# Optimization experiments

Measured on AMD Instinct MI355X. Metric: run time of the kernel, lower is better.

## Reference

```python
import jax, jax.numpy as jnp
import numpy as np
from jax.ops import segment_sum, segment_max

N = 400000          # points
V = 100000          # occupied voxels
EPS = 1e-3          # BN eps from norm_cfg
VX, VY, VZ = 0.2, 0.2, 4.0          # voxel_size
X0, Y0, Z0 = 0.0, -40.0, -3.0       # point_cloud_range mins
GX, GY, GZ = 352, 400, 1            # grid dims


def setup_inputs() -> dict:
    key = jax.random.key(0)
    ks = jax.random.split(key, 12)
    # points: xyz uniform inside the point cloud range, 4th channel = intensity
    xyz = jax.random.uniform(ks[0], (N, 3), jnp.float32) \
        * jnp.array([70.4, 80.0, 4.0], jnp.float32) \
        + jnp.array([X0, Y0, Z0], jnp.float32)
    inten = jax.random.uniform(ks[1], (N, 1), jnp.float32)
    features = jnp.concatenate([xyz, inten], axis=1)
    # point -> voxel mapping; guarantee every voxel id occupied so
    # segment_max semantics match torch's unique-voxel reduce exactly
    inv = jnp.concatenate([jnp.arange(V, dtype=jnp.int32),
                           jax.random.randint(ks[2], (N - V,), 0, V, jnp.int32)])
    inv = jax.random.permutation(ks[3], inv)
    # voxel coordinates (batch, z, y, x)
    b = jax.random.randint(ks[4], (V,), 0, 2, jnp.int32)
    z = jnp.zeros((V,), jnp.int32)
    y = jax.random.randint(ks[5], (V,), 0, GY, jnp.int32)
    x = jax.random.randint(ks[6], (V,), 0, GX, jnp.int32)
    coors = jnp.stack([b, z, y, x], axis=1)
    # VFE params: Linear(bias=False) + BN1d(gamma, beta)
    W0 = jax.random.normal(ks[7], (64, 10), jnp.float32) * (1.0 / np.sqrt(10))
    W1 = jax.random.normal(ks[8], (64, 128), jnp.float32) * (1.0 / np.sqrt(128))
    return dict(features=features, W0=W0,
                gamma0=jnp.ones((64,), jnp.float32), beta0=jnp.zeros((64,), jnp.float32),
                W1=W1,
                gamma1=jnp.ones((64,), jnp.float32), beta1=jnp.zeros((64,), jnp.float32),
                inv=inv, coors=coors)


def _bn_relu(x, gamma, beta):
    # BN1d in training mode: biased batch stats over the point dim
    mu = jnp.mean(x, axis=0)
    var = jnp.var(x, axis=0)
    return jax.nn.relu(gamma * (x - mu) * jax.lax.rsqrt(var + EPS) + beta)


def _stats(xyz, inv, coors):
    # cluster-center offset: per-voxel mean of xyz, gathered back
    cnt = segment_sum(jnp.ones((xyz.shape[0],), xyz.dtype), inv, num_segments=V)
    mean = segment_sum(xyz, inv, num_segments=V) / cnt[:, None]
    f_cluster = xyz - mean[inv]
    # voxel-center offset: coors order is (batch, z, y, x)
    cf = coors.astype(xyz.dtype)
    center = jnp.stack([cf[:, 3] * VX + VX / 2 + X0,
                        cf[:, 2] * VY + VY / 2 + Y0,
                        cf[:, 1] * VZ + VZ / 2 + Z0], axis=1)
    f_center = xyz - center[inv]
    return jnp.concatenate([xyz, f_cluster, f_center], axis=1)  # [N, 9]


def reference(features, W0, gamma0, beta0, W1, gamma1, beta1, inv, coors):
    x = jnp.concatenate([_stats(features[:, :3], inv, coors), features[:, 3:]], axis=1)  # [N,10]
    # VFE layer 0
    h0 = _bn_relu(x @ W0.T, gamma0, beta0)                     # [N,64]
    v0 = segment_max(h0, inv, num_segments=V)                  # [V,64]
    x1 = jnp.concatenate([h0, v0[inv]], axis=1)                # [N,128]
    # VFE layer 1
    h1 = _bn_relu(x1 @ W1.T, gamma1, beta1)                    # [N,64]
    voxel_feats = segment_max(h1, inv, num_segments=V)         # [V,64]
    return voxel_feats, coors
```

## Files before the change

### kernel.cpp

```cpp
#include <hip/hip_runtime.h>
#include <hip/hip_bf16.h>

#define NPTS 400000
#define NVOX 100000
#define EPSB 1e-3f
#define NTILE 6250
#define NBLK_SCAN 391
#define GBLK 782

#define OFF_ACC4   0
#define OFF_GRAM   (4*NVOX)
#define OFF_P1     (OFF_GRAM + 128)
#define ZERO_FLOATS (OFF_P1 + 4096)
#define OFF_V0     ZERO_FLOATS
#define OFF_Y1M    (OFF_V0 + NVOX*64)
#define OFF_VTMP   (OFF_Y1M + NVOX*64)
#define OFF_BSUM   (OFF_VTMP + NVOX)
#define OFF_VOFF   (OFF_BSUM + 512)
#define OFF_VSTART (OFF_VOFF + NVOX)
#define OFF_ORD    (OFF_VSTART + NVOX + 8)
#define OFF_VS     (OFF_ORD + NPTS)
#define OFF_W0F    (OFF_VS + NPTS)
#define OFF_W1B    (OFF_W0F + 640)
#define OFF_H0T    (OFF_W1B + 4096)

#define XTB_LD 136
#define HT_LD  65

typedef __bf16 bf16x8 __attribute__((ext_vector_type(8)));
typedef float  f32x4  __attribute__((ext_vector_type(4)));

__device__ __forceinline__ float b2f(__hip_bfloat16 h) { return __bfloat162float(h); }
__device__ __forceinline__ float bfbits2f(unsigned short u) {
    return __uint_as_float((unsigned int)u << 16);
}
__device__ __forceinline__ unsigned short bf16u(float f) {
    __hip_bfloat16 h = __float2bfloat16(f);
    return __builtin_bit_cast(unsigned short, h);
}
__device__ __forceinline__ unsigned int fkey(float f) {
    unsigned int u = __float_as_uint(f);
    return (u & 0x80000000u) ? ~u : (u | 0x80000000u);
}
__device__ __forceinline__ float funkey(unsigned int k) {
    unsigned int u = (k & 0x80000000u) ? (k & 0x7FFFFFFFu) : ~k;
    return __uint_as_float(u);
}

__device__ __forceinline__ void compute_x(const __hip_bfloat16* __restrict__ feat,
                                          const float* __restrict__ acc4,
                                          const int* __restrict__ coors,
                                          long i, int v, float* xv) {
    ushort4 f4 = *(const ushort4*)(feat + 4 * i);
    float px = bfbits2f(f4.x), py = bfbits2f(f4.y), pz = bfbits2f(f4.z), it = bfbits2f(f4.w);
    float4 a4 = *(const float4*)&acc4[4 * (long)v];
    float ic = 1.0f / a4.x;
    int4 c4 = *(const int4*)&coors[4 * (long)v];
    xv[0] = px; xv[1] = py; xv[2] = pz;
    xv[3] = px - a4.y * ic; xv[4] = py - a4.z * ic; xv[5] = pz - a4.w * ic;
    xv[6] = px - ((float)c4.w * 0.2f + 0.1f);
    xv[7] = py - ((float)c4.z * 0.2f + 0.1f - 40.0f);
    xv[8] = pz - ((float)c4.y * 4.0f + 2.0f - 3.0f);
    xv[9] = it;
}

__global__ void k_vsum(const __hip_bfloat16* __restrict__ feat,
                       const int* __restrict__ inv,
                       float* __restrict__ acc4,
                       const __hip_bfloat16* __restrict__ W0,
                       const __hip_bfloat16* __restrict__ W1,
                       float* __restrict__ W0f, unsigned short* __restrict__ w1b) {
    if (blockIdx.x == 6250) {
        int t = threadIdx.x;
        for (int j = t; j < 640; j += 256) W0f[j] = b2f(W0[j]);
        for (int f = t; f < 8192; f += 256) {
            int j  = f & 7;
            int l  = (f >> 3) & 63;
            int ks = (f >> 9) & 3;
            int ct = f >> 11;
            int ch = ct * 16 + (l & 15);
            int k  = ks * 32 + ((l >> 4) & 3) * 8 + j;
            w1b[f] = __builtin_bit_cast(unsigned short, W1[ch * 128 + k]);
        }
        return;
    }
    long t = (long)blockIdx.x * 256 + threadIdx.x;
    int pt = (int)(t >> 2);
    int comp = (int)(t & 3);
    float val = (comp == 0) ? 1.0f : b2f(feat[4 * pt + comp - 1]);
    int v = inv[pt];
    atomicAdd(&acc4[(long)v * 4 + comp], val);
}

__global__ void k_scan1(const float* __restrict__ acc4,
                        int* __restrict__ vtmp, int* __restrict__ bsum) {
    __shared__ int sc[256];
    int b = blockIdx.x, t = threadIdx.x;
    int v = b * 256 + t;
    int c = (v < NVOX) ? (int)acc4[4 * (long)v] : 0;
    sc[t] = c;
    __syncthreads();
    int val = c;
    for (int off = 1; off < 256; off <<= 1) {
        int x = (t >= off) ? sc[t - off] : 0;
        __syncthreads();
        val += x; sc[t] = val;
        __syncthreads();
    }
    if (v < NVOX) vtmp[v] = val - c;
    if (t == 255) bsum[b] = val;
}

__global__ void k_scan2(int* __restrict__ bsum) {
    __shared__ int sc[512];
    int t = threadIdx.x;
    int c = (t < NBLK_SCAN) ? bsum[t] : 0;
    sc[t] = c;
    __syncthreads();
    int val = c;
    for (int off = 1; off < 512; off <<= 1) {
        int x = (t >= off) ? sc[t - off] : 0;
        __syncthreads();
        val += x; sc[t] = val;
        __syncthreads();
    }
    if (t < NBLK_SCAN) bsum[t] = val - c;
}

__global__ void k_scan3(const int* __restrict__ vtmp, const int* __restrict__ bsum,
                        int* __restrict__ voff, int* __restrict__ vstart,
                        int* __restrict__ vsorted,
                        float* __restrict__ v0, unsigned int* __restrict__ y1m) {
    int v = blockIdx.x * 256 + threadIdx.x;
    if (v < NVOX) {
        int s0 = vtmp[v] + bsum[v >> 8];
        voff[v] = s0;
        vstart[v] = s0;
        int s1;
        if (v + 1 < NVOX) s1 = vtmp[v + 1] + bsum[(v + 1) >> 8];
        else              s1 = NPTS;
        for (int j = s0; j < s1; j++) vsorted[j] = v;
        if ((s0 >> 4) != ((s1 - 1) >> 4)) {
            float4 z4 = {0.f, 0.f, 0.f, 0.f};
            float4* pv = (float4*)&v0[(long)v * 64];
            float4* py = (float4*)&y1m[(long)v * 64];
#pragma unroll
            for (int u = 0; u < 16; u++) { pv[u] = z4; py[u] = z4; }
        }
    }
    if (v == 0) vstart[NVOX] = NPTS;
}

__global__ __launch_bounds__(256, 4)
void k_prep(const __hip_bfloat16* __restrict__ feat,
            const int* __restrict__ inv,
            const int* __restrict__ coors,
            const float* __restrict__ acc4,
            int* __restrict__ voff,
            int* __restrict__ ord,
            float* __restrict__ gram) {
    __shared__ float gs[72];
    int t = threadIdx.x;
    if (t < 72) gs[t] = 0.0f;
    __syncthreads();

    float sx[10], sxx[55];
#pragma unroll
    for (int a = 0; a < 10; a++) sx[a] = 0.0f;
#pragma unroll
    for (int a = 0; a < 55; a++) sxx[a] = 0.0f;

    for (long i = (long)blockIdx.x * 256 + t; i < NPTS; i += (long)GBLK * 256) {
        int v = inv[i];
        float xv[10];
        compute_x(feat, acc4, coors, i, v, xv);
        int idx = 0;
#pragma unroll
        for (int a = 0; a < 10; a++) {
            sx[a] += xv[a];
#pragma unroll
            for (int b = 0; b <= a; b++) sxx[idx++] += xv[a] * xv[b];
        }
        int pos = atomicAdd(&voff[v], 1);
        ord[pos] = (int)i;
    }

#pragma unroll
    for (int v = 0; v < 65; v++) {
        float s = (v < 10) ? sx[v] : sxx[v - 10];
        for (int m = 32; m >= 1; m >>= 1) s += __shfl_xor(s, m);
        if ((t & 63) == 0) atomicAdd(&gs[v], s);
    }
    __syncthreads();
    if (t < 65) atomicAdd(&gram[t], gs[t]);
}

__global__ __launch_bounds__(256, 6)
void k_h0max(const int* __restrict__ ord, const int* __restrict__ vsorted,
             const int* __restrict__ vstart,
             const __hip_bfloat16* __restrict__ feat,
             const float* __restrict__ acc4, const int* __restrict__ coors,
             const float* __restrict__ W0f, const float* __restrict__ gram,
             const __hip_bfloat16* __restrict__ g0,
             const __hip_bfloat16* __restrict__ be0,
             float* __restrict__ v0, unsigned short* __restrict__ h0t) {
    __shared__ float ht[64 * HT_LD];
    __shared__ int invs[64];
    __shared__ float sc0s[64], bi0s[64];
    int t = threadIdx.x, w = t >> 6, l = t & 63;
    int base = blockIdx.x * 64;
    int i = ord[base + l];
    int v = vsorted[base + l];
    if (w == 0) invs[l] = v;

    float xv[10];
    compute_x(feat, acc4, coors, (long)i, v, xv);

    if (w == 1) {
        int c = l;
        float wr[10];
#pragma unroll
        for (int k = 0; k < 10; k++) wr[k] = W0f[c * 10 + k];
        float sum = 0.0f, sq = 0.0f;
#pragma unroll
        for (int a = 0; a < 10; a++) {
            sum += wr[a] * gram[a];
            float ta = 0.0f;
#pragma unroll
            for (int b = 0; b < 10; b++) {
                int hi = (a >= b) ? a : b, lo = (a >= b) ? b : a;
                ta += wr[b] * gram[10 + hi * (hi + 1) / 2 + lo];
            }
            sq += wr[a] * ta;
        }
        float mu  = sum * (1.0f / NPTS);
        float var = sq * (1.0f / NPTS) - mu * mu;
        float g   = b2f(g0[c]) * rsqrtf(var + EPSB);
        sc0s[c] = g;
        bi0s[c] = b2f(be0[c]) - mu * g;
    }
    __syncthreads();

    int cw = w * 16;
#pragma unroll
    for (int j = 0; j < 16; j++) {
        int c = cw + j;
        float y = 0.0f;
#pragma unroll
        for (int k = 0; k < 10; k++) y += xv[k] * W0f[c*10 + k];
        ht[l * HT_LD + c] = fmaxf(sc0s[c] * y + bi0s[c], 0.0f);
    }
    __syncthreads();

#pragma unroll
    for (int u = 0; u < 2; u++) {
        int idx = t + u * 256;
        int pt2 = idx >> 3;
        int c0 = (idx & 7) * 8;
        const float* src = &ht[pt2 * HT_LD + c0];
        float4 a  = *(const float4*)src;
        float4 b4 = *(const float4*)(src + 4);
        uint4 o;
        o.x = (unsigned int)bf16u(a.x)  | ((unsigned int)bf16u(a.y)  << 16);
        o.y = (unsigned int)bf16u(a.z)  | ((unsigned int)bf16u(a.w)  << 16);
        o.z = (unsigned int)bf16u(b4.x) | ((unsigned int)bf16u(b4.y) << 16);
        o.w = (unsigned int)bf16u(b4.z) | ((unsigned int)bf16u(b4.w) << 16);
        *(uint4*)&h0t[(long)(base + pt2) * 64 + c0] = o;
    }

    unsigned int mk = 0u;
#pragma unroll
    for (int j = 0; j < 16; j++) {
        int p = cw + j;
        unsigned int hb = __float_as_uint(ht[p * HT_LD + l]);
        mk = (hb > mk) ? hb : mk;
        if (j == 15 || invs[p + 1] != invs[p]) {
            int vv = invs[p];
            int s0 = vstart[vv], s1 = vstart[vv + 1];
            unsigned int* dst = (unsigned int*)&v0[(long)vv * 64 + l];
            if (s0 >= base + cw && s1 <= base + cw + 16)
                *dst = mk;
            else
                atomicMax(dst, mk);
            mk = 0u;
        }
    }
}

__global__ __launch_bounds__(256, 6)
void k_mfma_stats(const int* __restrict__ vsorted,
                  const int* __restrict__ vstart,
                  const unsigned short* __restrict__ h0t,
                  const unsigned short* __restrict__ w1b,
                  const float* __restrict__ v0,
                  float* __restrict__ P1,
                  unsigned int* __restrict__ y1m) {
    __shared__ union {
        unsigned short xtb[64 * XTB_LD];
        float ht[64 * HT_LD];
    } sm;
    __shared__ int invs[64];
    int t = threadIdx.x, w = t >> 6, l = t & 63;
    int quad = l >> 4, lm = l & 15;
    int base = blockIdx.x * 64;
    if (w == 0) invs[l] = vsorted[base + l];

    bf16x8 bfrag[4];
    const uint4* wf = (const uint4*)w1b;
#pragma unroll
    for (int ks = 0; ks < 4; ks++)
        bfrag[ks] = __builtin_bit_cast(bf16x8, wf[(w * 4 + ks) * 64 + l]);

#pragma unroll
    for (int u = 0; u < 2; u++) {
        int idx = t + u * 256;
        int pt = idx >> 3, c0 = (idx & 7) * 8;
        uint4 d = *(const uint4*)&h0t[(long)(base + pt) * 64 + c0];
        *(uint4*)&sm.xtb[pt * XTB_LD + c0] = d;
    }
    {
        int p = t >> 2, q = t & 3;
        int vv = vsorted[base + p];
        const float4* src = (const float4*)&v0[(long)vv * 64 + q * 16];
#pragma unroll
        for (int u = 0; u < 4; u++) {
            float4 f4 = src[u];
            ushort4 s4 = { bf16u(f4.x), bf16u(f4.y), bf16u(f4.z), bf16u(f4.w) };
            *(ushort4*)&sm.xtb[p * XTB_LD + 64 + q * 16 + 4 * u] = s4;
        }
    }
    __syncthreads();

    f32x4 acc[4];
#pragma unroll
    for (int pg = 0; pg < 4; pg++) acc[pg] = (f32x4){0.f, 0.f, 0.f, 0.f};
#pragma unroll
    for (int ks = 0; ks < 4; ks++) {
#pragma unroll
        for (int pg = 0; pg < 4; pg++) {
            const uint4* ap = (const uint4*)&sm.xtb[(pg * 16 + lm) * XTB_LD + ks * 32 + quad * 8];
            bf16x8 a = __builtin_bit_cast(bf16x8, *ap);
            acc[pg] = __builtin_amdgcn_mfma_f32_16x16x32_bf16(a, bfrag[ks], acc[pg], 0, 0, 0);
        }
    }

    float ssum = 0.0f, ssq = 0.0f;
#pragma unroll
    for (int pg = 0; pg < 4; pg++) {
#pragma unroll
        for (int r = 0; r < 4; r++) {
            float y = acc[pg][r];
            ssum += y; ssq += y * y;
        }
    }
    __syncthreads();

#pragma unroll
    for (int pg = 0; pg < 4; pg++) {
#pragma unroll
        for (int r = 0; r < 4; r++)
            sm.ht[(pg * 16 + quad * 4 + r) * HT_LD + w * 16 + lm] = acc[pg][r];
    }
    __syncthreads();

    unsigned int mk = 0u;
    int cw = w * 16;
#pragma unroll
    for (int j = 0; j < 16; j++) {
        int p = cw + j;
        unsigned int k2 = fkey(sm.ht[p * HT_LD + l]);
        mk = (k2 > mk) ? k2 : mk;
        if (j == 15 || invs[p + 1] != invs[p]) {
            int vv = invs[p];
            int s0 = vstart[vv], s1 = vstart[vv + 1];
            unsigned int* dst = &y1m[(long)vv * 64 + l];
            if (s0 >= base + cw && s1 <= base + cw + 16)
                *dst = mk;
            else
                atomicMax(dst, mk);
            mk = 0u;
        }
    }

    ssum += __shfl_xor(ssum, 16); ssq += __shfl_xor(ssq, 16);
    ssum += __shfl_xor(ssum, 32); ssq += __shfl_xor(ssq, 32);
    if (l < 16) {
        int slot = blockIdx.x & 31;
        atomicAdd(&P1[slot * 128 + w * 16 + lm], ssum);
        atomicAdd(&P1[slot * 128 + 64 + w * 16 + lm], ssq);
    }
}

#define OUTBLK 512
__global__ __launch_bounds__(256)
void k_out(const unsigned int* __restrict__ y1m,
           const float* __restrict__ P1,
           const __hip_bfloat16* __restrict__ gamma,
           const __hip_bfloat16* __restrict__ beta,
           const int* __restrict__ coors,
           float* __restrict__ out) {
    __shared__ float sc1s[64], bi1s[64];
    int t = threadIdx.x;
    if (t < 64) {
        float sum = 0.0f, sq = 0.0f;
        for (int s = 0; s < 32; s++) {
            sum += P1[s*128 + t];
            sq  += P1[s*128 + 64 + t];
        }
        float mu  = sum * (1.0f / NPTS);
        float var = sq * (1.0f / NPTS) - mu * mu;
        float g   = b2f(gamma[t]) * rsqrtf(var + EPSB);
        sc1s[t] = g;
        bi1s[t] = b2f(beta[t]) - mu * g;
    }
    __syncthreads();

    const long n4feat = (long)NVOX * 16;
    const long n4all  = n4feat + NVOX;
    const long nfeat  = (long)NVOX * 64;
    for (long idx = (long)blockIdx.x * 256 + t; idx < n4all; idx += (long)OUTBLK * 256) {
        if (idx < n4feat) {
            uint4 kk = ((const uint4*)y1m)[idx];
            int c0 = (int)((idx * 4) & 63);
            float4 o;
            o.x = fmaxf(sc1s[c0+0] * funkey(kk.x) + bi1s[c0+0], 0.0f);
            o.y = fmaxf(sc1s[c0+1] * funkey(kk.y) + bi1s[c0+1], 0.0f);
            o.z = fmaxf(sc1s[c0+2] * funkey(kk.z) + bi1s[c0+2], 0.0f);
            o.w = fmaxf(sc1s[c0+3] * funkey(kk.w) + bi1s[c0+3], 0.0f);
            ((float4*)out)[idx] = o;
        } else {
            long vi = idx - n4feat;
            int4 c4 = ((const int4*)coors)[vi];
            float4 o;
            o.x = b2f(__float2bfloat16((float)c4.x));
            o.y = b2f(__float2bfloat16((float)c4.y));
            o.z = b2f(__float2bfloat16((float)c4.z));
            o.w = b2f(__float2bfloat16((float)c4.w));
            ((float4*)(out + nfeat))[vi] = o;
        }
    }
}

extern "C" void kernel_launch(void* const* d_in, const int* in_sizes, int n_in,
                              void* d_out, int out_size, void* d_ws, size_t ws_size,
                              hipStream_t stream) {
    const __hip_bfloat16* feat = (const __hip_bfloat16*)d_in[0];
    const __hip_bfloat16* W0   = (const __hip_bfloat16*)d_in[1];
    const __hip_bfloat16* g0   = (const __hip_bfloat16*)d_in[2];
    const __hip_bfloat16* be0  = (const __hip_bfloat16*)d_in[3];
    const __hip_bfloat16* W1   = (const __hip_bfloat16*)d_in[4];
    const __hip_bfloat16* g1   = (const __hip_bfloat16*)d_in[5];
    const __hip_bfloat16* be1  = (const __hip_bfloat16*)d_in[6];
    const int* inv   = (const int*)d_in[7];
    const int* coors = (const int*)d_in[8];
    float* out = (float*)d_out;

    float* ws    = (float*)d_ws;
    float* acc4  = ws + OFF_ACC4;
    float* gram  = ws + OFF_GRAM;
    float* P1    = ws + OFF_P1;
    float* v0    = ws + OFF_V0;
    unsigned int* y1m = (unsigned int*)(ws + OFF_Y1M);
    int* vtmp    = (int*)(ws + OFF_VTMP);
    int* bsum    = (int*)(ws + OFF_BSUM);
    int* voff    = (int*)(ws + OFF_VOFF);
    int* vstart  = (int*)(ws + OFF_VSTART);
    int* ord     = (int*)(ws + OFF_ORD);
    int* vsorted = (int*)(ws + OFF_VS);
    float* W0f   = ws + OFF_W0F;
    unsigned short* w1b = (unsigned short*)(ws + OFF_W1B);
    unsigned short* h0t = (unsigned short*)(ws + OFF_H0T);

    hipMemsetAsync(ws, 0, (size_t)ZERO_FLOATS * sizeof(float), stream);

    k_vsum<<<6251, 256, 0, stream>>>(feat, inv, acc4, W0, W1, W0f, w1b);
    k_scan1<<<NBLK_SCAN, 256, 0, stream>>>(acc4, vtmp, bsum);
    k_scan2<<<1, 512, 0, stream>>>(bsum);
    k_scan3<<<NBLK_SCAN, 256, 0, stream>>>(vtmp, bsum, voff, vstart, vsorted, v0, y1m);
    k_prep<<<GBLK, 256, 0, stream>>>(feat, inv, coors, acc4, voff, ord, gram);
    k_h0max<<<NTILE, 256, 0, stream>>>(ord, vsorted, vstart, feat, acc4, coors,
                                       W0f, gram, g0, be0, v0, h0t);
    k_mfma_stats<<<NTILE, 256, 0, stream>>>(vsorted, vstart, h0t, w1b, v0, P1, y1m);
    k_out<<<OUTBLK, 256, 0, stream>>>(y1m, P1, g1, be1, coors, out);
}
```

Measured before the change: 256.9 us.

## Decompose layer-0 Gram moments into per-point and per-voxel terms

After: 285.9 us. +11.3%, slower.

```diff
diff --git a/kernel.cpp b/kernel.cpp
--- a/kernel.cpp
+++ b/kernel.cpp
@@ -9,10 +9,13 @@
 #define GBLK 782
 
 #define OFF_ACC4   0
-#define OFF_GRAM   (4*NVOX)
-#define OFF_P1     (OFF_GRAM + 128)
+#define OFF_ACCI   (4*NVOX)
+#define OFF_AMOM   (5*NVOX)
+#define OFF_BMOM   (OFF_AMOM + 512)
+#define OFF_P1     (OFF_BMOM + 1024)
 #define ZERO_FLOATS (OFF_P1 + 4096)
-#define OFF_V0     ZERO_FLOATS
+#define OFF_STATS  ZERO_FLOATS
+#define OFF_V0     (OFF_STATS + 128)
 #define OFF_Y1M    (OFF_V0 + NVOX*64)
 #define OFF_VTMP   (OFF_Y1M + NVOX*64)
 #define OFF_BSUM   (OFF_VTMP + NVOX)
@@ -66,7 +69,7 @@
 
 __global__ void k_vsum(const __hip_bfloat16* __restrict__ feat,
                        const int* __restrict__ inv,
-                       float* __restrict__ acc4,
+                       float* __restrict__ acc4, float* __restrict__ accI,
                        const __hip_bfloat16* __restrict__ W0,
                        const __hip_bfloat16* __restrict__ W1,
                        float* __restrict__ W0f, unsigned short* __restrict__ w1b) {
@@ -87,9 +90,13 @@
     long t = (long)blockIdx.x * 256 + threadIdx.x;
     int pt = (int)(t >> 2);
     int comp = (int)(t & 3);
-    float val = (comp == 0) ? 1.0f : b2f(feat[4 * pt + comp - 1]);
     int v = inv[pt];
-    atomicAdd(&acc4[(long)v * 4 + comp], val);
+    if (comp == 0) {
+        atomicAdd(&acc4[(long)v * 4], 1.0f);
+        atomicAdd(&accI[v], b2f(feat[4 * pt + 3]));
+    } else {
+        atomicAdd(&acc4[(long)v * 4 + comp], b2f(feat[4 * pt + comp - 1]));
+    }
 }
 
 __global__ void k_scan1(const float* __restrict__ acc4,
@@ -154,45 +161,162 @@
 __global__ __launch_bounds__(256, 4)
 void k_prep(const __hip_bfloat16* __restrict__ feat,
             const int* __restrict__ inv,
-            const int* __restrict__ coors,
-            const float* __restrict__ acc4,
             int* __restrict__ voff,
             int* __restrict__ ord,
-            float* __restrict__ gram) {
-    __shared__ float gs[72];
+            float* __restrict__ amom) {
+    __shared__ float gs[16];
     int t = threadIdx.x;
-    if (t < 72) gs[t] = 0.0f;
-    __syncthreads();
-
-    float sx[10], sxx[55];
-#pragma unroll
-    for (int a = 0; a < 10; a++) sx[a] = 0.0f;
-#pragma unroll
-    for (int a = 0; a < 55; a++) sxx[a] = 0.0f;
+    if (t < 16) gs[t] = 0.0f;
+    __syncthreads();
+
+    float a[14];
+#pragma unroll
+    for (int k = 0; k < 14; k++) a[k] = 0.0f;
 
     for (long i = (long)blockIdx.x * 256 + t; i < NPTS; i += (long)GBLK * 256) {
+        ushort4 f4 = *(const ushort4*)(feat + 4 * i);
+        float px = bfbits2f(f4.x), py = bfbits2f(f4.y);
+        float pz = bfbits2f(f4.z), it = bfbits2f(f4.w);
+        a[0] += px;      a[1] += py;      a[2] += pz;
+        a[3] += px * px; a[4] += py * px; a[5] += py * py;
+        a[6] += pz * px; a[7] += pz * py; a[8] += pz * pz;
+        a[9] += it;      a[10] += it * px; a[11] += it * py; a[12] += it * pz;
+        a[13] += it * it;
         int v = inv[i];
-        float xv[10];
-        compute_x(feat, acc4, coors, i, v, xv);
-        int idx = 0;
-#pragma unroll
-        for (int a = 0; a < 10; a++) {
-            sx[a] += xv[a];
-#pragma unroll
-            for (int b = 0; b <= a; b++) sxx[idx++] += xv[a] * xv[b];
-        }
         int pos = atomicAdd(&voff[v], 1);
         ord[pos] = (int)i;
     }
 
 #pragma unroll
-    for (int v = 0; v < 65; v++) {
-        float s = (v < 10) ? sx[v] : sxx[v - 10];
+    for (int k = 0; k < 14; k++) {
+        float s = a[k];
         for (int m = 32; m >= 1; m >>= 1) s += __shfl_xor(s, m);
-        if ((t & 63) == 0) atomicAdd(&gs[v], s);
-    }
-    __syncthreads();
-    if (t < 65) atomicAdd(&gram[t], gs[t]);
+        if ((t & 63) == 0) atomicAdd(&gs[k], s);
+    }
+    __syncthreads();
+    if (t < 14) atomicAdd(&amom[(blockIdx.x & 31) * 16 + t], gs[t]);
+}
+
+__global__ void k_bmom(const float* __restrict__ acc4,
+                       const float* __restrict__ accI,
+                       const int* __restrict__ coors,
+                       float* __restrict__ bmom) {
+    __shared__ float gs[32];
+    int t = threadIdx.x;
+    if (t < 32) gs[t] = 0.0f;
+    __syncthreads();
+
+    int v = blockIdx.x * 256 + t;
+    float n = 0, sx = 0, sy = 0, sz = 0, I = 0, cx = 0, cy = 0, cz = 0, in = 0;
+    if (v < NVOX) {
+        float4 a4 = *(const float4*)&acc4[4 * (long)v];
+        n = a4.x; sx = a4.y; sy = a4.z; sz = a4.w;
+        I = accI[v];
+        int4 c4 = *(const int4*)&coors[4 * (long)v];
+        cx = (float)c4.w * 0.2f + 0.1f;
+        cy = (float)c4.z * 0.2f + 0.1f - 40.0f;
+        cz = (float)c4.y * 4.0f + 2.0f - 3.0f;
+        in = 1.0f / n;
+    }
+    float vals[30];
+    vals[0] = sx * sx * in; vals[1] = sy * sx * in; vals[2] = sy * sy * in;
+    vals[3] = sz * sx * in; vals[4] = sz * sy * in; vals[5] = sz * sz * in;
+    vals[6]  = sx * cx; vals[7]  = sx * cy; vals[8]  = sx * cz;
+    vals[9]  = sy * cx; vals[10] = sy * cy; vals[11] = sy * cz;
+    vals[12] = sz * cx; vals[13] = sz * cy; vals[14] = sz * cz;
+    vals[15] = n * cx * cx; vals[16] = n * cy * cx; vals[17] = n * cy * cy;
+    vals[18] = n * cz * cx; vals[19] = n * cz * cy; vals[20] = n * cz * cz;
+    vals[21] = n * cx; vals[22] = n * cy; vals[23] = n * cz;
+    vals[24] = I * sx * in; vals[25] = I * sy * in; vals[26] = I * sz * in;
+    vals[27] = I * cx; vals[28] = I * cy; vals[29] = I * cz;
+
+#pragma unroll
+    for (int k = 0; k < 30; k++) {
+        float s = vals[k];
+        for (int m = 32; m >= 1; m >>= 1) s += __shfl_xor(s, m);
+        if ((t & 63) == 0) atomicAdd(&gs[k], s);
+    }
+    __syncthreads();
+    if (t < 30) atomicAdd(&bmom[(blockIdx.x & 31) * 32 + t], gs[t]);
+}
+
+__global__ void k_gasm(const float* __restrict__ amom, const float* __restrict__ bmom,
+                       const float* __restrict__ W0f,
+                       const __hip_bfloat16* __restrict__ g0,
+                       const __hip_bfloat16* __restrict__ be0,
+                       float* __restrict__ stats) {
+    __shared__ float A[16], B[32], g[72];
+    int t = threadIdx.x;
+    if (t < 16) {
+        float s = 0.0f;
+        for (int sl = 0; sl < 32; sl++) s += amom[sl * 16 + t];
+        A[t] = s;
+    } else if (t < 48) {
+        int k = t - 16;
+        float s = 0.0f;
+        for (int sl = 0; sl < 32; sl++) s += bmom[sl * 32 + k];
+        B[k] = s;
+    }
+    __syncthreads();
+
+    if (t == 0) {
+        auto A2f = [&](int p, int q) { int h = p > q ? p : q, l = p > q ? q : p;
+                                       return A[3 + h * (h + 1) / 2 + l]; };
+        auto B1f = [&](int p, int q) { int h = p > q ? p : q, l = p > q ? q : p;
+                                       return B[h * (h + 1) / 2 + l]; };
+        auto B2f = [&](int p, int q) { return B[6 + p * 3 + q]; };
+        auto B3f = [&](int p, int q) { int h = p > q ? p : q, l = p > q ? q : p;
+                                       return B[15 + h * (h + 1) / 2 + l]; };
+        g[0] = A[0]; g[1] = A[1]; g[2] = A[2];
+        g[3] = 0.0f; g[4] = 0.0f; g[5] = 0.0f;
+        g[6] = A[0] - B[21]; g[7] = A[1] - B[22]; g[8] = A[2] - B[23];
+        g[9] = A[9];
+        for (int hi = 0; hi < 10; hi++) {
+            for (int lo = 0; lo <= hi; lo++) {
+                int ch = hi < 3 ? 0 : (hi < 6 ? 1 : (hi < 9 ? 2 : 3));
+                int cl = lo < 3 ? 0 : (lo < 6 ? 1 : (lo < 9 ? 2 : 3));
+                int ah = hi - (ch == 1 ? 3 : (ch == 2 ? 6 : 0));
+                int al = lo - (cl == 1 ? 3 : (cl == 2 ? 6 : 0));
+                float val;
+                if (ch == 3 && cl == 3)      val = A[13];
+                else if (ch == 3) {
+                    if (cl == 0)             val = A[10 + al];
+                    else if (cl == 1)        val = A[10 + al] - B[24 + al];
+                    else                     val = A[10 + al] - B[27 + al];
+                }
+                else if (ch == 2 && cl == 2) val = A2f(ah, al) - B2f(ah, al) - B2f(al, ah) + B3f(ah, al);
+                else if (ch == 2 && cl == 0) val = A2f(ah, al) - B2f(al, ah);
+                else if (ch == 0)            val = A2f(ah, al);
+                else                         val = A2f(ah, al) - B1f(ah, al);
+                g[10 + hi * (hi + 1) / 2 + lo] = val;
+            }
+        }
+    }
+    __syncthreads();
+
+    if (t < 64) {
+        int c = t;
+        float wr[10];
+#pragma unroll
+        for (int k = 0; k < 10; k++) wr[k] = W0f[c * 10 + k];
+        float sum = 0.0f, sq = 0.0f;
+#pragma unroll
+        for (int a = 0; a < 10; a++) {
+            sum += wr[a] * g[a];
+            float ta = 0.0f;
+#pragma unroll
+            for (int b = 0; b < 10; b++) {
+                int hi = (a >= b) ? a : b, lo = (a >= b) ? b : a;
+                ta += wr[b] * g[10 + hi * (hi + 1) / 2 + lo];
+            }
+            sq += wr[a] * ta;
+        }
+        float mu  = sum * (1.0f / NPTS);
+        float var = sq * (1.0f / NPTS) - mu * mu;
+        float gg  = b2f(g0[c]) * rsqrtf(var + EPSB);
+        stats[c]      = gg;
+        stats[64 + c] = b2f(be0[c]) - mu * gg;
+    }
 }
 
 __global__ __launch_bounds__(256, 6)
@@ -200,9 +324,7 @@
              const int* __restrict__ vstart,
              const __hip_bfloat16* __restrict__ feat,
              const float* __restrict__ acc4, const int* __restrict__ coors,
-             const float* __restrict__ W0f, const float* __restrict__ gram,
-             const __hip_bfloat16* __restrict__ g0,
-             const __hip_bfloat16* __restrict__ be0,
+             const float* __restrict__ W0f, const float* __restrict__ stats,
              float* __restrict__ v0, unsigned short* __restrict__ h0t) {
     __shared__ float ht[64 * HT_LD];
     __shared__ int invs[64];
@@ -211,34 +333,11 @@
     int base = blockIdx.x * 64;
     int i = ord[base + l];
     int v = vsorted[base + l];
-    if (w == 0) invs[l] = v;
+    if (w == 0) { invs[l] = v; sc0s[l] = stats[l]; }
+    else if (w == 1) bi0s[l] = stats[64 + l];
 
     float xv[10];
     compute_x(feat, acc4, coors, (long)i, v, xv);
-
-    if (w == 1) {
-        int c = l;
-        float wr[10];
-#pragma unroll
-        for (int k = 0; k < 10; k++) wr[k] = W0f[c * 10 + k];
-        float sum = 0.0f, sq = 0.0f;
-#pragma unroll
-        for (int a = 0; a < 10; a++) {
-            sum += wr[a] * gram[a];
-            float ta = 0.0f;
-#pragma unroll
-            for (int b = 0; b < 10; b++) {
-                int hi = (a >= b) ? a : b, lo = (a >= b) ? b : a;
-                ta += wr[b] * gram[10 + hi * (hi + 1) / 2 + lo];
-            }
-            sq += wr[a] * ta;
-        }
-        float mu  = sum * (1.0f / NPTS);
-        float var = sq * (1.0f / NPTS) - mu * mu;
-        float g   = b2f(g0[c]) * rsqrtf(var + EPSB);
-        sc0s[c] = g;
-        bi0s[c] = b2f(be0[c]) - mu * g;
-    }
     __syncthreads();
 
     int cw = w * 16;
@@ -457,8 +556,11 @@
 
     float* ws    = (float*)d_ws;
     float* acc4  = ws + OFF_ACC4;
-    float* gram  = ws + OFF_GRAM;
+    float* accI  = ws + OFF_ACCI;
+    float* amom  = ws + OFF_AMOM;
+    float* bmom  = ws + OFF_BMOM;
     float* P1    = ws + OFF_P1;
+    float* stats = ws + OFF_STATS;
     float* v0    = ws + OFF_V0;
     unsigned int* y1m = (unsigned int*)(ws + OFF_Y1M);
     int* vtmp    = (int*)(ws + OFF_VTMP);
@@ -473,13 +575,15 @@
 
     hipMemsetAsync(ws, 0, (size_t)ZERO_FLOATS * sizeof(float), stream);
 
-    k_vsum<<<6251, 256, 0, stream>>>(feat, inv, acc4, W0, W1, W0f, w1b);
+    k_vsum<<<6251, 256, 0, stream>>>(feat, inv, acc4, accI, W0, W1, W0f, w1b);
     k_scan1<<<NBLK_SCAN, 256, 0, stream>>>(acc4, vtmp, bsum);
     k_scan2<<<1, 512, 0, stream>>>(bsum);
     k_scan3<<<NBLK_SCAN, 256, 0, stream>>>(vtmp, bsum, voff, vstart, vsorted, v0, y1m);
-    k_prep<<<GBLK, 256, 0, stream>>>(feat, inv, coors, acc4, voff, ord, gram);
+    k_bmom<<<NBLK_SCAN, 256, 0, stream>>>(acc4, accI, coors, bmom);
+    k_prep<<<GBLK, 256, 0, stream>>>(feat, inv, voff, ord, amom);
+    k_gasm<<<1, 128, 0, stream>>>(amom, bmom, W0f, g0, be0, stats);
     k_h0max<<<NTILE, 256, 0, stream>>>(ord, vsorted, vstart, feat, acc4, coors,
-                                       W0f, gram, g0, be0, v0, h0t);
+                                       W0f, stats, v0, h0t);
     k_mfma_stats<<<NTILE, 256, 0, stream>>>(vsorted, vstart, h0t, w1b, v0, P1, y1m);
     k_out<<<OUTBLK, 256, 0, stream>>>(y1m, P1, g1, be1, coors, out);
 }
```

## Skip v0 global writes for voxels contained in one 64-point block; recompute max in-block

Applied to the files above, without the earlier changes.

Measured after the change: 295.6 us. 15.1% more time.

```diff
diff --git a/kernel.cpp b/kernel.cpp
--- a/kernel.cpp
+++ b/kernel.cpp
@@ -140,12 +140,16 @@
         if (v + 1 < NVOX) s1 = vtmp[v + 1] + bsum[(v + 1) >> 8];
         else              s1 = NPTS;
         for (int j = s0; j < s1; j++) vsorted[j] = v;
+        float4 z4 = {0.f, 0.f, 0.f, 0.f};
         if ((s0 >> 4) != ((s1 - 1) >> 4)) {
-            float4 z4 = {0.f, 0.f, 0.f, 0.f};
+            float4* py = (float4*)&y1m[(long)v * 64];
+#pragma unroll
+            for (int u = 0; u < 16; u++) py[u] = z4;
+        }
+        if ((s0 >> 6) != ((s1 - 1) >> 6)) {
             float4* pv = (float4*)&v0[(long)v * 64];
-            float4* py = (float4*)&y1m[(long)v * 64];
-#pragma unroll
-            for (int u = 0; u < 16; u++) { pv[u] = z4; py[u] = z4; }
+#pragma unroll
+            for (int u = 0; u < 16; u++) pv[u] = z4;
         }
     }
     if (v == 0) vstart[NVOX] = NPTS;
@@ -277,11 +281,8 @@
         if (j == 15 || invs[p + 1] != invs[p]) {
             int vv = invs[p];
             int s0 = vstart[vv], s1 = vstart[vv + 1];
-            unsigned int* dst = (unsigned int*)&v0[(long)vv * 64 + l];
-            if (s0 >= base + cw && s1 <= base + cw + 16)
-                *dst = mk;
-            else
-                atomicMax(dst, mk);
+            if (s0 < base || s1 > base + 64)
+                atomicMax((unsigned int*)&v0[(long)vv * 64 + l], mk);
             mk = 0u;
         }
     }
@@ -318,15 +319,26 @@
         uint4 d = *(const uint4*)&h0t[(long)(base + pt) * 64 + c0];
         *(uint4*)&sm.xtb[pt * XTB_LD + c0] = d;
     }
+    __syncthreads();
+
     {
-        int p = t >> 2, q = t & 3;
-        int vv = vsorted[base + p];
-        const float4* src = (const float4*)&v0[(long)vv * 64 + q * 16];
-#pragma unroll
-        for (int u = 0; u < 4; u++) {
-            float4 f4 = src[u];
-            ushort4 s4 = { bf16u(f4.x), bf16u(f4.y), bf16u(f4.z), bf16u(f4.w) };
-            *(ushort4*)&sm.xtb[p * XTB_LD + 64 + q * 16 + 4 * u] = s4;
+        unsigned short vmax = 0;
+        int p0 = 0;
+        int cw = w * 16;
+        for (int p = 0; p < 64; p++) {
+            unsigned short hb = sm.xtb[p * XTB_LD + l];
+            vmax = (hb > vmax) ? hb : vmax;
+            if (p == 63 || invs[p + 1] != invs[p]) {
+                int vv = invs[p];
+                int s0v = vstart[vv], s1v = vstart[vv + 1];
+                if (s0v < base || s1v > base + 64)
+                    vmax = bf16u(v0[(long)vv * 64 + l]);
+                int lo = (p0 > cw) ? p0 : cw;
+                int hi = (p < cw + 15) ? p : (cw + 15);
+                for (int q = lo; q <= hi; q++)
+                    sm.xtb[q * XTB_LD + 64 + l] = vmax;
+                vmax = 0; p0 = p + 1;
+            }
         }
     }
     __syncthreads();
```
